# Optimization experiments

Measured on AMD Instinct MI355X. Metric: run time of the kernel, lower is better.

The kernel has to match this reference:

```python
import jax, jax.numpy as jnp
import numpy as np

INPUT_SIZE = 1024
OUTPUT_SIZE = 1024
B, S = 4, 2048


def setup_inputs() -> dict:
    key = jax.random.key(0)
    k1, k2, k3, k4, k5, k6 = jax.random.split(key, 6)
    scale = 1.0 / np.sqrt(INPUT_SIZE)
    return {
        "inputs_for_keys": jax.random.normal(k1, (B, S, INPUT_SIZE), jnp.float32),
        "inputs_for_values": jax.random.normal(k2, (B, S, INPUT_SIZE), jnp.float32),
        "inputs_for_queries": jax.random.normal(k3, (B, S, INPUT_SIZE), jnp.float32),
        "W_k": jax.random.normal(k4, (INPUT_SIZE, OUTPUT_SIZE), jnp.float32) * scale,
        "W_v": jax.random.normal(k5, (INPUT_SIZE, OUTPUT_SIZE), jnp.float32) * scale,
        "W_q": jax.random.normal(k6, (INPUT_SIZE, OUTPUT_SIZE), jnp.float32) * scale,
    }


def reference(inputs_for_keys, inputs_for_values, inputs_for_queries, W_k, W_v, W_q):
    # Linear projections (bias=False): x @ W  -> [B, S, D_out]
    K = jnp.einsum("bsi,io->bso", inputs_for_keys, W_k)
    V = jnp.einsum("bsi,io->bso", inputs_for_values, W_v)
    Q = jnp.einsum("bqi,io->bqo", inputs_for_queries, W_q)
    d_k = K.shape[-1]
    # scores: [B, Sq, Sk], scaled by sqrt(embedding_size of K)
    scores = jnp.einsum("bqd,bkd->bqk", Q, K) / jnp.sqrt(jnp.asarray(d_k, Q.dtype))
    # causal mask: positions k > q masked to -inf (use_mask=True since is_self_attention)
    q_idx = jnp.arange(Q.shape[1])[:, None]
    k_idx = jnp.arange(K.shape[1])[None, :]
    scores = jnp.where(k_idx > q_idx, jnp.asarray(-jnp.inf, scores.dtype), scores)
    weights = jax.nn.softmax(scores, axis=-1)
    # output: [B, Sq, D_out]
    return jnp.einsum("bqk,bkd->bqd", weights, V)
```

## Files before the change

kernel.cpp:

```cpp
#include <hip/hip_runtime.h>


typedef __attribute__((ext_vector_type(8))) short short8;
typedef __attribute__((ext_vector_type(4))) float floatx4;

static constexpr long long XE = 8388608LL;
static constexpr long long WE = 1048576LL;

static __device__ __forceinline__ unsigned short f2b(float f) {
  unsigned u = __builtin_bit_cast(unsigned, f);
  u = (u + 0x7fffu + ((u >> 16) & 1u)) >> 16;
  return (unsigned short)u;
}

static __device__ __forceinline__ void gload16(const unsigned short* g, unsigned short* l) {
  __builtin_amdgcn_global_load_lds(
      (const __attribute__((address_space(1))) unsigned int*)g,
      (__attribute__((address_space(3))) unsigned int*)l, 16, 0, 0);
}

template <int NF>
static __device__ __forceinline__ void gemm_loop(
    const unsigned short* __restrict__ A, const unsigned short* __restrict__ Bt,
    int lda, int ldb, int nk, int bi, int bj,
    unsigned short* lA, unsigned short* lB, floatx4 acc[4][NF]) {
  const int t = threadIdx.x, wave = t >> 6, lane = t & 63;
  const int wr = wave >> 1, wc = wave & 1;
  const int sr = lane >> 3;
  const int sc = ((lane & 7) ^ sr) * 8;
  const unsigned short* gA = A + (long long)(bi * 128 + wave * 32 + sr) * lda + sc;
  const unsigned short* gB = Bt + (long long)(bj * (NF * 32) + wave * (NF * 8) + sr) * ldb + sc;
  unsigned short* lAw = lA + wave * 2048;
  unsigned short* lBw = lB + wave * (NF * 512);
  const int frow = lane & 15, hi = lane >> 4;

  for (int ks = 0; ks < nk; ++ks) {
    const long long k0 = (long long)ks * 64;
    __syncthreads();
#pragma unroll
    for (int g = 0; g < 4; ++g)
      gload16(gA + (long long)g * 8 * lda + k0, lAw + g * 512);
#pragma unroll
    for (int g = 0; g < NF; ++g)
      gload16(gB + (long long)g * 8 * ldb + k0, lBw + g * 512);
    __syncthreads();
#pragma unroll
    for (int kk = 0; kk < 2; ++kk) {
      const int ch = (kk * 4 + hi) ^ (frow & 7);
      short8 af[4], bf[NF];
#pragma unroll
      for (int m = 0; m < 4; ++m)
        af[m] = *(const short8*)&lA[(wr * 64 + m * 16 + frow) * 64 + ch * 8];
#pragma unroll
      for (int n = 0; n < NF; ++n)
        bf[n] = *(const short8*)&lB[(wc * (NF * 16) + n * 16 + frow) * 64 + ch * 8];
#pragma unroll
      for (int m = 0; m < 4; ++m)
#pragma unroll
        for (int n = 0; n < NF; ++n)
          acc[m][n] = __builtin_amdgcn_mfma_f32_16x16x32_bf16(af[m], bf[n], acc[m][n], 0, 0, 0);
    }
  }
}

__global__ __launch_bounds__(256) void gt_kernel(
    const unsigned short* __restrict__ WkB, const unsigned short* __restrict__ WqB,
    unsigned short* __restrict__ Gt) {
  __shared__ __align__(16) unsigned short lA[8192], lB[8192];
  floatx4 acc[4][4] = {};
  gemm_loop<4>(WkB, WqB, 1024, 1024, 16, blockIdx.x, blockIdx.y, lA, lB, acc);
  const int tid = threadIdx.x, wave = tid >> 6, lane = tid & 63;
  const int wr = wave >> 1, wc = wave & 1, frow = lane & 15, hi = lane >> 4;
  const long long crow0 = (long long)blockIdx.x * 128 + wr * 64 + hi * 4;
  const int ccol = blockIdx.y * 128 + wc * 64 + frow;
#pragma unroll
  for (int m = 0; m < 4; ++m)
#pragma unroll
    for (int j = 0; j < 4; ++j) {
      unsigned short* cp = Gt + (crow0 + m * 16 + j) * 1024 + ccol;
#pragma unroll
      for (int n = 0; n < 4; ++n) cp[n * 16] = f2b(acc[m][n][j]);
    }
}

__global__ __launch_bounds__(256) void projTV(
    const unsigned short* __restrict__ Xb, const unsigned short* __restrict__ WvT,
    const unsigned short* __restrict__ Gt, unsigned short* __restrict__ Tb,
    unsigned short* __restrict__ Vt) {
  __shared__ __align__(16) unsigned short lA[8192], lB[8192];
  const int orig = blockIdx.x;
  const int w = (orig & 7) * 128 + (orig >> 3);
  const unsigned short *A, *B;
  unsigned short* C;
  int ldc, bi, bj;
  if (w < 512) { A = Xb + XE; B = Gt; C = Tb; ldc = 1024; bi = w >> 3; bj = w & 7; }
  else { const int j = w - 512; A = WvT; B = Xb; C = Vt; ldc = 8192; bi = j & 7; bj = j >> 3; }
  floatx4 acc[4][4] = {};
  gemm_loop<4>(A, B, 1024, 1024, 16, bi, bj, lA, lB, acc);
  const int tid = threadIdx.x, wave = tid >> 6, lane = tid & 63;
  const int wr = wave >> 1, wc = wave & 1, frow = lane & 15, hi = lane >> 4;
  const long long crow0 = (long long)bi * 128 + wr * 64 + hi * 4;
  const int ccol = bj * 128 + wc * 64 + frow;
#pragma unroll
  for (int m = 0; m < 4; ++m)
#pragma unroll
    for (int j = 0; j < 4; ++j) {
      unsigned short* cp = C + (crow0 + m * 16 + j) * (long long)ldc + ccol;
#pragma unroll
      for (int n = 0; n < 4; ++n) cp[n * 16] = f2b(acc[m][n][j]);
    }
}

__global__ __launch_bounds__(256) void scores_exp(
    const unsigned short* __restrict__ Tb, const unsigned short* __restrict__ Xk,
    unsigned short* __restrict__ P, float* __restrict__ Rpart) {
  __shared__ __align__(16) unsigned short lA[8192], lB[4096];
  const int orig = blockIdx.x;
  const int w = (orig & 7) * 136 + (orig >> 3);
  const int b = w / 272;
  int t2 = w - b * 272;
  int bi = 0;
  while (t2 >= 2 * bi + 2) { t2 -= 2 * bi + 2; ++bi; }
  const int bj = t2;

  floatx4 acc[4][2] = {};
  gemm_loop<2>(Tb + (long long)b * 2048 * 1024, Xk + (long long)b * 2048 * 1024,
               1024, 1024, 16, bi, bj, lA, lB, acc);

  const int tid = threadIdx.x, wave = tid >> 6, lane = tid & 63;
  const int wr = wave >> 1, wc = wave & 1, frow = lane & 15, hi = lane >> 4;
  const bool diag = (bj >= 2 * bi);
  float rp[4][4];
#pragma unroll
  for (int m = 0; m < 4; ++m)
#pragma unroll
    for (int j = 0; j < 4; ++j) {
      const int rloc = wr * 64 + hi * 4 + m * 16 + j;
      const int rglob = bi * 128 + rloc;
      float s = 0.f;
#pragma unroll
      for (int n = 0; n < 2; ++n) {
        const int cglob = bj * 64 + wc * 32 + n * 16 + frow;
        float e = __expf(acc[m][n][j] * 0.03125f);
        if (diag && cglob > rglob) e = 0.f;
        acc[m][n][j] = e;
        s += e;
      }
      rp[m][j] = s;
    }
#pragma unroll
  for (int m = 0; m < 4; ++m)
#pragma unroll
    for (int j = 0; j < 4; ++j) {
      rp[m][j] += __shfl_xor(rp[m][j], 1);
      rp[m][j] += __shfl_xor(rp[m][j], 2);
      rp[m][j] += __shfl_xor(rp[m][j], 4);
      rp[m][j] += __shfl_xor(rp[m][j], 8);
    }
  unsigned short* C = P + (long long)b * 2048 * 2048;
  const long long crow0 = (long long)bi * 128 + wr * 64 + hi * 4;
  const int ccol = bj * 64 + wc * 32 + frow;
#pragma unroll
  for (int m = 0; m < 4; ++m)
#pragma unroll
    for (int j = 0; j < 4; ++j) {
      unsigned short* cp = C + (crow0 + m * 16 + j) * 2048LL + ccol;
      cp[0] = f2b(acc[m][0][j]);
      cp[16] = f2b(acc[m][1][j]);
    }
  __syncthreads();
  float* red = (float*)lA;
  if (frow == 0) {
#pragma unroll
    for (int m = 0; m < 4; ++m)
#pragma unroll
      for (int j = 0; j < 4; ++j)
        red[(wr * 64 + hi * 4 + m * 16 + j) * 2 + wc] = rp[m][j];
  }
  __syncthreads();
  if (tid < 128)
    Rpart[((long long)b * 32 + bj) * 2048 + bi * 128 + tid] = red[tid * 2] + red[tid * 2 + 1];
}

__global__ __launch_bounds__(256) void rowsum(
    const float* __restrict__ Rpart, float* __restrict__ Rinv) {
  const int t = blockIdx.x * 256 + threadIdx.x;
  const int b = t >> 11, row = t & 2047;
  const int nb = (row >> 6) + 1;
  float s = 0.f;
  for (int bj = 0; bj < nb; ++bj) s += Rpart[(b * 32 + bj) * 2048 + row];
  Rinv[t] = 1.f / s;
}

__global__ __launch_bounds__(256) void pv_kernel(
    const unsigned short* __restrict__ P, const unsigned short* __restrict__ Vt,
    const float* __restrict__ Rinv, float* __restrict__ out) {
  __shared__ __align__(16) unsigned short lA[8192], lB[4096];
  const int orig = blockIdx.x;
  const int w = (orig & 7) * 128 + (orig >> 3);
  const int tt = w >> 1, s = w & 1;
  const int p = tt & 7;
  const int bi = s ? 15 - p : p;
  const int b = (tt >> 3) & 3;
  const int bj = tt >> 5;
  floatx4 acc[4][2] = {};
  gemm_loop<2>(P + (long long)b * 2048 * 2048, Vt + (long long)b * 2048, 2048, 8192,
               (bi + 1) * 2, bi, bj, lA, lB, acc);
  const int tid = threadIdx.x, wave = tid >> 6, lane = tid & 63;
  const int wr = wave >> 1, wc = wave & 1, frow = lane & 15, hi = lane >> 4;
  float* C = out + (long long)b * 2048 * 1024;
  const float* Ri = Rinv + b * 2048;
#pragma unroll
  for (int m = 0; m < 4; ++m)
#pragma unroll
    for (int j = 0; j < 4; ++j) {
      const int row = bi * 128 + wr * 64 + hi * 4 + m * 16 + j;
      const float riv = Ri[row];
      float* cp = C + (long long)row * 1024 + bj * 64 + wc * 32 + frow;
      cp[0] = acc[m][0][j] * riv;
      cp[16] = acc[m][1][j] * riv;
    }
}

__global__ __launch_bounds__(256) void cvtAll(
    const float* __restrict__ Xk, const float* __restrict__ Xv,
    const float* __restrict__ Xq, const float* __restrict__ Wq,
    const float* __restrict__ Wk, const float* __restrict__ Wv,
    unsigned short* __restrict__ Xb, unsigned short* __restrict__ WqB,
    unsigned short* __restrict__ WkB, unsigned short* __restrict__ WvT) {
  __shared__ unsigned short tile[64][65];
  const int bx = blockIdx.x, t = threadIdx.x;
  if (bx < 3072) {
    const int y = bx >> 10, sub = bx & 1023;
    const float* in = y == 0 ? Xv : (y == 1 ? Xq : Xk);
    unsigned short* o = Xb + (long long)y * XE;
    const int n4 = (int)(XE / 4), stride = 1024 * 256;
    for (int i = sub * 256 + t; i < n4; i += stride) {
      float4 x = ((const float4*)in)[i];
      ushort4 v;
      v.x = f2b(x.x); v.y = f2b(x.y); v.z = f2b(x.z); v.w = f2b(x.w);
      ((ushort4*)o)[i] = v;
    }
  } else if (bx < 3328) {
    const int w2 = bx - 3072;
    const int y = w2 >> 7, sub = w2 & 127;
    const float* in = y == 0 ? Wq : Wk;
    unsigned short* o = y == 0 ? WqB : WkB;
    const int n4 = (int)(WE / 4), stride = 128 * 256;
    for (int i = sub * 256 + t; i < n4; i += stride) {
      float4 x = ((const float4*)in)[i];
      ushort4 v;
      v.x = f2b(x.x); v.y = f2b(x.y); v.z = f2b(x.z); v.w = f2b(x.w);
      ((ushort4*)o)[i] = v;
    }
  } else {
    const int v = bx - 3328;
    const int i0 = (v & 15) * 64, j0 = (v >> 4) * 64;
#pragma unroll
    for (int r = 0; r < 16; ++r) {
      int lin = r * 256 + t;
      int i = lin >> 6, j = lin & 63;
      tile[i][j] = f2b(Wv[(long long)(i0 + i) * 1024 + j0 + j]);
    }
    __syncthreads();
#pragma unroll
    for (int r = 0; r < 16; ++r) {
      int lin = r * 256 + t;
      int o = lin >> 6, i = lin & 63;
      WvT[(long long)(j0 + o) * 1024 + i0 + i] = tile[i][o];
    }
  }
}

extern "C" void kernel_launch(void* const* d_in, const int* in_sizes, int n_in,
                              void* d_out, int out_size, void* d_ws, size_t ws_size,
                              hipStream_t stream) {
  const float* Xk = (const float*)d_in[0];
  const float* Xv = (const float*)d_in[1];
  const float* Xq = (const float*)d_in[2];
  const float* Wk = (const float*)d_in[3];
  const float* Wv = (const float*)d_in[4];
  const float* Wq = (const float*)d_in[5];
  float* out = (float*)d_out;

  unsigned short* ws = (unsigned short*)d_ws;
  unsigned short* Xb = ws;
  unsigned short* WqB = ws + 3 * XE;
  unsigned short* WkB = WqB + WE;
  unsigned short* WvT = WkB + WE;
  unsigned short* Gt = WvT + WE;
  unsigned short* Tb = Gt + WE;
  unsigned short* Vt = Tb + XE;
  float* Rpart = (float*)(Vt + XE);
  float* Rinv = Rpart + 4 * 32 * 2048;
  unsigned short* Pbuf = ws;

  cvtAll<<<3584, 256, 0, stream>>>(Xk, Xv, Xq, Wq, Wk, Wv, Xb, WqB, WkB, WvT);
  gt_kernel<<<dim3(8, 8), 256, 0, stream>>>(WkB, WqB, Gt);
  projTV<<<1024, 256, 0, stream>>>(Xb, WvT, Gt, Tb, Vt);
  scores_exp<<<1088, 256, 0, stream>>>(Tb, Xb + 2 * XE, Pbuf, Rpart);
  rowsum<<<32, 256, 0, stream>>>(Rpart, Rinv);
  pv_kernel<<<1024, 256, 0, stream>>>(Pbuf, Vt, Rinv, out);
}
```

Baseline: 179.5 us.

## Replace projection GEMM with 256x256-tile 8-wave double-buffered kernel

Replaces the 128x128-tile projTV GEMM (1024 blocks of 256 threads) with projTV8, which uses 256x256 output tiles, 512 threads, and 128 KB of dynamic LDS double-buffered with interleaved global-to-LDS staging and MFMA phases. The goal is higher arithmetic intensity per tile and overlap of global loads with matrix math, cutting memory traffic and stalls in the projection stage. The cost is much larger shared memory per block and only 256 blocks, which lowers occupancy and may leave CUs underused. The hand-placed waitcnt and barrier scheduling is also fragile.

Result: faster. 169.9 us (-5.4%).

```diff
diff --git a/kernel.cpp b/kernel.cpp
--- a/kernel.cpp
+++ b/kernel.cpp
@@ -17,6 +17,136 @@
   __builtin_amdgcn_global_load_lds(
       (const __attribute__((address_space(1))) unsigned int*)g,
       (__attribute__((address_space(3))) unsigned int*)l, 16, 0, 0);
+}
+
+#define VMCNT(n) asm volatile("s_waitcnt vmcnt(" #n ")" ::: "memory")
+#define LGKM0() asm volatile("s_waitcnt lgkmcnt(0)" ::: "memory")
+#define BARRIER() do { asm volatile("" ::: "memory"); __builtin_amdgcn_s_barrier(); asm volatile("" ::: "memory"); } while (0)
+
+
+#define STAGE(base, matoff, h, slot, kt) do {                                  \
+    const unsigned short* _s = (base) + (h) * 131072 + (kt) * 64;              \
+    char* _d = sb + (slot) * 65536 + (matoff) + (h) * 16384 + dwave;           \
+    gload16(_s, (unsigned short*)_d);                                          \
+    gload16(_s + 65536, (unsigned short*)(_d + 8192));                         \
+  } while (0)
+
+#define READ_A(slot, mb) do {                                                  \
+    const char* _p = sb + (slot) * 65536 + aoffb + (mb) * 2048;                \
+    af[0][0] = *(const short8*)(_p + c0);        af[0][1] = *(const short8*)(_p + c1); \
+    af[1][0] = *(const short8*)(_p + 2048 + c0); af[1][1] = *(const short8*)(_p + 2048 + c1); \
+    af[2][0] = *(const short8*)(_p + 4096 + c0); af[2][1] = *(const short8*)(_p + 4096 + c1); \
+    af[3][0] = *(const short8*)(_p + 6144 + c0); af[3][1] = *(const short8*)(_p + 6144 + c1); \
+  } while (0)
+
+#define READ_B(slot, nb, bfx) do {                                             \
+    const char* _p = sb + (slot) * 65536 + boffb + (nb) * 2048;                \
+    bfx[0][0] = *(const short8*)(_p + c0);        bfx[0][1] = *(const short8*)(_p + c1); \
+    bfx[1][0] = *(const short8*)(_p + 2048 + c0); bfx[1][1] = *(const short8*)(_p + 2048 + c1); \
+  } while (0)
+
+#define MF16(MB, NB, bfx) do {                                                 \
+    __builtin_amdgcn_s_setprio(1);                                             \
+    _Pragma("unroll")                                                          \
+    for (int _m = 0; _m < 4; ++_m) {                                           \
+      _Pragma("unroll")                                                        \
+      for (int _n = 0; _n < 2; ++_n) {                                         \
+        acc[(MB) + _m][(NB) + _n] = __builtin_amdgcn_mfma_f32_16x16x32_bf16(   \
+            af[_m][0], bfx[_n][0], acc[(MB) + _m][(NB) + _n], 0, 0, 0);        \
+        acc[(MB) + _m][(NB) + _n] = __builtin_amdgcn_mfma_f32_16x16x32_bf16(   \
+            af[_m][1], bfx[_n][1], acc[(MB) + _m][(NB) + _n], 0, 0, 0);        \
+      } }                                                                      \
+    __builtin_amdgcn_s_setprio(0);                                             \
+  } while (0)
+
+__global__ __launch_bounds__(512, 2) void projTV8(
+    const unsigned short* __restrict__ Xb, const unsigned short* __restrict__ WvT,
+    const unsigned short* __restrict__ Gt, unsigned short* __restrict__ Tb,
+    unsigned short* __restrict__ Vt) {
+  extern __shared__ char sb[];
+  const int orig = blockIdx.x;
+  const int w = (orig & 7) * 32 + (orig >> 3);
+  const unsigned short *Aop, *Bop;
+  unsigned short* C;
+  int ldc, bi, bj;
+  if (w < 128) { Aop = Xb + XE; Bop = Gt; C = Tb; ldc = 1024; bi = w >> 2; bj = w & 3; }
+  else { const int j = w - 128; Aop = WvT; Bop = Xb; C = Vt; ldc = 8192; bi = j & 3; bj = j >> 2; }
+
+  const int tid = threadIdx.x, wave = tid >> 6, lane = tid & 63;
+  const int wm = wave >> 2, wn = wave & 3, frow = lane & 15, hi = lane >> 4;
+  const int r0 = tid >> 3, p0 = ((tid & 7) ^ (r0 & 7)) * 8;
+  const int dwave = wave * 1024;
+  const int sx = frow & 7;
+  const int c0 = (hi ^ sx) * 16, c1 = ((4 + hi) ^ sx) * 16;
+  const int aoffb = (wm * 128 + frow) * 128;
+  const int boffb = 32768 + (wn * 64 + frow) * 128;
+  const unsigned short* Ab = Aop + (long long)(bi * 256 + r0) * 1024 + p0;
+  const unsigned short* Bb = Bop + (long long)(bj * 256 + r0) * 1024 + p0;
+
+  short8 af[4][2], bf0[2][2], bf1[2][2];
+  floatx4 acc[8][4] = {};
+
+  STAGE(Ab, 0, 0, 0, 0);     STAGE(Ab, 0, 1, 0, 0);
+  STAGE(Bb, 32768, 0, 0, 0); STAGE(Bb, 32768, 1, 0, 0);
+  STAGE(Bb, 32768, 0, 1, 1); STAGE(Bb, 32768, 1, 1, 1);
+  VMCNT(4);
+  BARRIER();
+
+  for (int t = 0; t < 8; ++t) {
+    const int kt1 = 2 * t + 1, kt2 = 2 * t + 2, kt3 = 2 * t + 3;
+    const bool pf = t < 7;
+    READ_A(0, 0); READ_B(0, 0, bf0);
+    STAGE(Ab, 0, 0, 1, kt1);
+    BARRIER(); LGKM0();
+    MF16(0, 0, bf0);
+    BARRIER();
+    READ_B(0, 2, bf1);
+    STAGE(Ab, 0, 1, 1, kt1);
+    BARRIER(); LGKM0();
+    MF16(0, 2, bf1);
+    BARRIER();
+    READ_A(0, 4);
+    if (pf) STAGE(Bb, 32768, 0, 0, kt2);
+    BARRIER(); LGKM0();
+    MF16(4, 2, bf1);
+    BARRIER();
+    if (pf) STAGE(Bb, 32768, 1, 0, kt2);
+    BARRIER();
+    MF16(4, 0, bf0);
+    if (pf) { VMCNT(4); } else { VMCNT(0); }
+    BARRIER();
+    READ_A(1, 0); READ_B(1, 0, bf0);
+    if (pf) STAGE(Ab, 0, 0, 0, kt2);
+    BARRIER(); LGKM0();
+    MF16(0, 0, bf0);
+    BARRIER();
+    READ_B(1, 2, bf1);
+    if (pf) STAGE(Ab, 0, 1, 0, kt2);
+    BARRIER(); LGKM0();
+    MF16(0, 2, bf1);
+    BARRIER();
+    READ_A(1, 4);
+    if (pf) STAGE(Bb, 32768, 0, 1, kt3);
+    BARRIER(); LGKM0();
+    MF16(4, 2, bf1);
+    BARRIER();
+    if (pf) STAGE(Bb, 32768, 1, 1, kt3);
+    BARRIER();
+    MF16(4, 0, bf0);
+    if (pf) { VMCNT(4); } else { VMCNT(0); }
+    BARRIER();
+  }
+
+  const long long crow0 = (long long)bi * 256 + wm * 128 + hi * 4;
+  const int ccol = bj * 256 + wn * 64 + frow;
+#pragma unroll
+  for (int m = 0; m < 8; ++m)
+#pragma unroll
+    for (int j = 0; j < 4; ++j) {
+      unsigned short* cp = C + (crow0 + m * 16 + j) * (long long)ldc + ccol;
+#pragma unroll
+      for (int n = 0; n < 4; ++n) cp[n * 16] = f2b(acc[m][j < 0 ? 0 : n][j]);
+    }
 }
 
 template <int NF>
@@ -78,34 +208,6 @@
 #pragma unroll
     for (int j = 0; j < 4; ++j) {
       unsigned short* cp = Gt + (crow0 + m * 16 + j) * 1024 + ccol;
-#pragma unroll
-      for (int n = 0; n < 4; ++n) cp[n * 16] = f2b(acc[m][n][j]);
-    }
-}
-
-__global__ __launch_bounds__(256) void projTV(
-    const unsigned short* __restrict__ Xb, const unsigned short* __restrict__ WvT,
-    const unsigned short* __restrict__ Gt, unsigned short* __restrict__ Tb,
-    unsigned short* __restrict__ Vt) {
-  __shared__ __align__(16) unsigned short lA[8192], lB[8192];
-  const int orig = blockIdx.x;
-  const int w = (orig & 7) * 128 + (orig >> 3);
-  const unsigned short *A, *B;
-  unsigned short* C;
-  int ldc, bi, bj;
-  if (w < 512) { A = Xb + XE; B = Gt; C = Tb; ldc = 1024; bi = w >> 3; bj = w & 7; }
-  else { const int j = w - 512; A = WvT; B = Xb; C = Vt; ldc = 8192; bi = j & 7; bj = j >> 3; }
-  floatx4 acc[4][4] = {};
-  gemm_loop<4>(A, B, 1024, 1024, 16, bi, bj, lA, lB, acc);
-  const int tid = threadIdx.x, wave = tid >> 6, lane = tid & 63;
-  const int wr = wave >> 1, wc = wave & 1, frow = lane & 15, hi = lane >> 4;
-  const long long crow0 = (long long)bi * 128 + wr * 64 + hi * 4;
-  const int ccol = bj * 128 + wc * 64 + frow;
-#pragma unroll
-  for (int m = 0; m < 4; ++m)
-#pragma unroll
-    for (int j = 0; j < 4; ++j) {
-      unsigned short* cp = C + (crow0 + m * 16 + j) * (long long)ldc + ccol;
 #pragma unroll
       for (int n = 0; n < 4; ++n) cp[n * 16] = f2b(acc[m][n][j]);
     }
@@ -297,7 +399,7 @@
 
   cvtAll<<<3584, 256, 0, stream>>>(Xk, Xv, Xq, Wq, Wk, Wv, Xb, WqB, WkB, WvT);
   gt_kernel<<<dim3(8, 8), 256, 0, stream>>>(WkB, WqB, Gt);
-  projTV<<<1024, 256, 0, stream>>>(Xb, WvT, Gt, Tb, Vt);
+  projTV8<<<256, 512, 131072, stream>>>(Xb, WvT, Gt, Tb, Vt);
   scores_exp<<<1088, 256, 0, stream>>>(Tb, Xb + 2 * XE, Pbuf, Rpart);
   rowsum<<<32, 256, 0, stream>>>(Rpart, Rinv);
   pv_kernel<<<1024, 256, 0, stream>>>(Pbuf, Vt, Rinv, out);
```
